# Kernel tuning notes

Hardware: AMD Instinct MI355X
Metric: run time of the kernel (lower is better)

Reference implementation:

```python
import jax, jax.numpy as jnp
import numpy as np

B = 65536
HID = 128
OUT = 10


def setup_inputs() -> dict:
    key = jax.random.key(0)
    ks = jax.random.split(key, 6)
    x = jax.random.normal(ks[0], (B, 784), dtype=jnp.float32)
    conv_w = jax.random.normal(ks[1], (3, 3), dtype=jnp.float32)
    # torch Linear(676,128): weight [128,676], bias [128]
    w1 = jax.random.normal(ks[2], (HID, 26 * 26), dtype=jnp.float32) * (1.0 / np.sqrt(26 * 26))
    b1 = jax.random.normal(ks[3], (HID,), dtype=jnp.float32) * 0.01
    w2 = jax.random.normal(ks[4], (OUT, HID), dtype=jnp.float32) * (1.0 / np.sqrt(HID))
    b2 = jax.random.normal(ks[5], (OUT,), dtype=jnp.float32) * 0.01
    return {"x": x, "conv_w": conv_w, "w1": w1, "b1": b1, "w2": w2, "b2": b2}


def reference(x, conv_w, w1, b1, w2, b2):
    b = x.shape[0]
    img = x.reshape(b, 1, 28, 28)                      # NCHW, single channel
    kern = conv_w.reshape(1, 1, 3, 3)                  # OIHW
    # valid 3x3 cross-correlation (matches the elementwise-multiply-and-sum loop)
    conv = jax.lax.conv_general_dilated(
        img, kern, window_strides=(1, 1), padding="VALID",
        dimension_numbers=("NCHW", "OIHW", "NCHW"))   # [B,1,26,26]
    feat = conv.reshape(b, 26 * 26)
    h = jax.nn.relu(feat @ w1.T + b1)                  # [B,128]
    return h @ w2.T + b2                               # [B,10]
```

## Files before the change

### kernel.cpp

```cpp
#include <hip/hip_runtime.h>
#include <hip/hip_bf16.h>

#define BATCH  65536
#define KREAL  784
#define BK     64
#define NCHUNK 13
#define HID    128
#define NOUT   10
#define BM     64
#define NTHR   256

using f32x4  = __attribute__((ext_vector_type(4))) float;
using short8 = __attribute__((ext_vector_type(8))) short;
using short4v= __attribute__((ext_vector_type(4))) short;
using f4     = __attribute__((ext_vector_type(4))) float;

__device__ inline short f2b(float f) {
    union { __hip_bfloat16 h; short s; } u;
    u.h = __float2bfloat16(f);
    return u.s;
}

#define GLDS16(gp, lp) \
    __builtin_amdgcn_global_load_lds((const __attribute__((address_space(1))) void*)(gp), \
                                     (__attribute__((address_space(3))) void*)(lp), 16, 0, 0)

#define NWB (NCHUNK*HID*BK)
#define NW2 (4*4*16*8)

__global__ void prep_kernel(const float* __restrict__ conv_w,
                            const float* __restrict__ w1,
                            const float* __restrict__ w2,
                            unsigned short* __restrict__ weff_sw,
                            unsigned short* __restrict__ w2f)
{
    int idx = blockIdx.x * 256 + threadIdx.x;
    if (idx < NWB) {
        int ic  = idx >> 13;
        int rem = idx & 8191;
        int r   = rem >> 6;
        int cc  = rem & 63;
        int g   = (cc >> 3) ^ (r & 7);
        int k   = ic * BK + g * 8 + (cc & 7);
        float acc = 0.f;
        if (k < KREAL) {
            int rr = k / 28, c = k - rr * 28;
            #pragma unroll
            for (int di = 0; di < 3; ++di) {
                int i = rr - di;
                if (i >= 0 && i < 26) {
                    #pragma unroll
                    for (int dj = 0; dj < 3; ++dj) {
                        int j = c - dj;
                        if (j >= 0 && j < 26)
                            acc = fmaf(w1[r * 676 + i * 26 + j], conv_w[di * 3 + dj], acc);
                    }
                }
            }
        }
        weff_sw[idx] = (unsigned short)f2b(acc);
    } else {
        int k2 = idx - NWB;
        if (k2 < NW2) {
            int e  = k2 & 7;
            int lo = (k2 >> 3) & 15;
            int hi = (k2 >> 7) & 3;
            int kk = k2 >> 9;
            float v = (lo < NOUT) ? w2[lo * HID + kk * 32 + hi * 8 + e] : 0.f;
            w2f[k2] = (unsigned short)f2b(v);
        }
    }
}

__global__ __launch_bounds__(NTHR, 4)
void fused_mlp_kernel(const float* __restrict__ x,
                      const float* __restrict__ b1,
                      const float* __restrict__ b2,
                      const unsigned short* __restrict__ weff_sw,
                      const unsigned short* __restrict__ w2f,
                      float* __restrict__ out)
{
    __shared__ __align__(16) unsigned char smem[40960];
    unsigned short* ldsA  = (unsigned short*)smem;
    unsigned short* ldsB0 = (unsigned short*)(smem + 8192);
    unsigned short* ldsB1 = (unsigned short*)(smem + 24576);
    unsigned short* ldsH  = (unsigned short*)smem;
    float*          outS  = (float*)(smem + 16384);

    const int tid  = threadIdx.x;
    const int wv   = tid >> 6;
    const int lane = tid & 63;
    const int lo   = lane & 15;
    const int hi   = lane >> 4;
    const int row0 = blockIdx.x * BM;
    const int wr0  = wv * 16;
    const int c0   = blockIdx.x % NCHUNK;

    f32x4 acc[8];
    #pragma unroll
    for (int t = 0; t < 8; ++t) acc[t] = (f32x4){0.f, 0.f, 0.f, 0.f};

    const char* abase = (const char*)(x + (long)(row0 + wr0 + hi) * KREAL);
    f4 av[4];
    auto issueA = [&](int ic) {
        #pragma unroll
        for (int j = 0; j < 4; ++j) {
            int ce = ic * BK + lo * 4;
            int cb = (ce + 4 <= KREAL) ? ce : 0;
            av[j] = *(const f4*)(abase + (long)j * 4 * KREAL * 4 + (long)cb * 4);
        }
    };
    auto writeA = [&]() {
        #pragma unroll
        for (int j = 0; j < 4; ++j) {
            int r = wr0 + j * 4 + hi;
            short4v c;
            c[0] = f2b(av[j][0]); c[1] = f2b(av[j][1]);
            c[2] = f2b(av[j][2]); c[3] = f2b(av[j][3]);
            int byteoff = r * 128 + ((((lo >> 1) ^ (r & 7)) << 4)) + ((lo & 1) << 3);
            *(short4v*)((char*)ldsA + byteoff) = c;
        }
    };
    auto stageB = [&](int ic, unsigned short* dst) {
        const char* src = (const char*)(weff_sw + (long)ic * (HID * BK));
        #pragma unroll
        for (int j = 0; j < 4; ++j)
            GLDS16(src + wv * 4096 + j * 1024 + lane * 16,
                   (char*)dst + wv * 4096 + j * 1024);
    };

    issueA(c0);
    stageB(c0, ldsB0);
    writeA();
    asm volatile("s_waitcnt vmcnt(0)" ::: "memory");
    __builtin_amdgcn_sched_barrier(0);
    __builtin_amdgcn_s_barrier();
    __builtin_amdgcn_sched_barrier(0);

    #pragma unroll
    for (int s = 0; s < NCHUNK; ++s) {
        int ic  = c0 + s;     if (ic >= NCHUNK)  ic -= NCHUNK;
        int icn = ic + 1;     if (icn >= NCHUNK) icn -= NCHUNK;
        const unsigned short* Bc = (s & 1) ? ldsB1 : ldsB0;
        if (s + 1 < NCHUNK) {
            issueA(icn);
            stageB(icn, (s & 1) ? ldsB0 : ldsB1);
        }
        const int r = wr0 + lo;
        #pragma unroll
        for (int kk = 0; kk < 2; ++kk) {
            const int G = kk * 4 + hi;
            short8 af = *(const short8*)((const char*)ldsA + r * 128 + ((G ^ (r & 7)) << 4));
            #pragma unroll
            for (int t = 0; t < 8; ++t) {
                const int ob = t * 16 + lo;
                short8 bfrag = *(const short8*)&Bc[ob * BK + ((G ^ (ob & 7)) << 3)];
                acc[t] = __builtin_amdgcn_mfma_f32_16x16x32_bf16(af, bfrag, acc[t], 0, 0, 0);
            }
        }
        if (s + 1 < NCHUNK) {
            __builtin_amdgcn_sched_barrier(0);
            writeA();
            __builtin_amdgcn_sched_barrier(0);
            asm volatile("s_waitcnt vmcnt(0)" ::: "memory");
            __builtin_amdgcn_sched_barrier(0);
            __builtin_amdgcn_s_barrier();
            __builtin_amdgcn_sched_barrier(0);
        }
    }

    __builtin_amdgcn_sched_barrier(0);
    __builtin_amdgcn_s_barrier();
    __builtin_amdgcn_sched_barrier(0);

    #pragma unroll
    for (int t = 0; t < 8; ++t) {
        float bias = b1[t * 16 + lo];
        #pragma unroll
        for (int j = 0; j < 4; ++j) {
            float hv = acc[t][j] + bias;
            hv = hv > 0.f ? hv : 0.f;
            int rloc = wr0 + hi * 4 + j;
            int col  = t * 16 + lo;
            int g    = col >> 3, e = col & 7;
            ldsH[rloc * HID + ((g ^ (rloc & 7)) << 3) + e] = (unsigned short)f2b(hv);
        }
    }

    f32x4 acc2 = (f32x4){0.f, 0.f, 0.f, 0.f};
    #pragma unroll
    for (int kk = 0; kk < 4; ++kk) {
        int r = wr0 + lo;
        int g = kk * 4 + hi;
        short8 ha = *(const short8*)&ldsH[r * HID + ((g ^ (r & 7)) << 3)];
        short8 wb = *(const short8*)(w2f + (((kk * 4 + hi) * 16 + lo) << 3));
        acc2 = __builtin_amdgcn_mfma_f32_16x16x32_bf16(ha, wb, acc2, 0, 0, 0);
    }
    float* os = outS + wv * 160;
    if (lo < NOUT) {
        float bb = b2[lo];
        #pragma unroll
        for (int j = 0; j < 4; ++j)
            os[(hi * 4 + j) * NOUT + lo] = acc2[j] + bb;
    }
    if (lane < 40) {
        f4 v = *(const f4*)&os[lane * 4];
        *(f4*)(out + (long)(row0 + wr0) * NOUT + lane * 4) = v;
    }
}

extern "C" void kernel_launch(void* const* d_in, const int* in_sizes, int n_in,
                              void* d_out, int out_size, void* d_ws, size_t ws_size,
                              hipStream_t stream)
{
    const float* x      = (const float*)d_in[0];
    const float* conv_w = (const float*)d_in[1];
    const float* w1     = (const float*)d_in[2];
    const float* b1     = (const float*)d_in[3];
    const float* w2     = (const float*)d_in[4];
    const float* b2     = (const float*)d_in[5];
    float* out = (float*)d_out;

    unsigned short* weff_sw = (unsigned short*)d_ws;
    unsigned short* w2f     = weff_sw + NWB;

    const int prep_total = NWB + NW2;
    prep_kernel<<<(prep_total + 255) / 256, 256, 0, stream>>>(conv_w, w1, w2, weff_sw, w2f);
    fused_mlp_kernel<<<BATCH / BM, NTHR, 0, stream>>>(x, b1, b2, weff_sw, w2f, out);
}
```

Baseline: 43.29 us.

## Split K across wave pairs with 512 threads and reduce partials in LDS

Doubles the block to 512 threads so each 16-row group is handled by two waves, each covering half of every 64-wide K chunk. The loads per thread for A and B staging are halved. At the end, one wave writes its partial hidden accumulators to LDS as bf16 and the other adds them before the bias, ReLU and the second layer. The goal is more waves in flight to hide memory latency. The cost is an extra LDS reduction and barrier, and bf16 rounding of the partial sums, which adds numerical error.

```diff
diff --git a/kernel.cpp b/kernel.cpp
--- a/kernel.cpp
+++ b/kernel.cpp
@@ -8,7 +8,7 @@
 #define HID    128
 #define NOUT   10
 #define BM     64
-#define NTHR   256
+#define NTHR   512
 
 using f32x4  = __attribute__((ext_vector_type(4))) float;
 using short8 = __attribute__((ext_vector_type(8))) short;
@@ -19,6 +19,10 @@
     union { __hip_bfloat16 h; short s; } u;
     u.h = __float2bfloat16(f);
     return u.s;
+}
+__device__ inline float b2f(unsigned short s) {
+    union { unsigned int u; float f; } c; c.u = ((unsigned int)s) << 16;
+    return c.f;
 }
 
 #define GLDS16(gp, lp) \
@@ -72,7 +76,7 @@
     }
 }
 
-__global__ __launch_bounds__(NTHR, 4)
+__global__ __launch_bounds__(NTHR, 7)
 void fused_mlp_kernel(const float* __restrict__ x,
                       const float* __restrict__ b1,
                       const float* __restrict__ b2,
@@ -85,48 +89,52 @@
     unsigned short* ldsB0 = (unsigned short*)(smem + 8192);
     unsigned short* ldsB1 = (unsigned short*)(smem + 24576);
     unsigned short* ldsH  = (unsigned short*)smem;
-    float*          outS  = (float*)(smem + 16384);
+    unsigned short* scrP  = (unsigned short*)(smem + 16384);
+    float*          outS  = (float*)(smem + 32768);
 
     const int tid  = threadIdx.x;
     const int wv   = tid >> 6;
     const int lane = tid & 63;
     const int lo   = lane & 15;
     const int hi   = lane >> 4;
+    const int g    = wv >> 1;
+    const int kh   = wv & 1;
     const int row0 = blockIdx.x * BM;
-    const int wr0  = wv * 16;
+    const int wr0  = g * 16;
     const int c0   = blockIdx.x % NCHUNK;
 
     f32x4 acc[8];
     #pragma unroll
     for (int t = 0; t < 8; ++t) acc[t] = (f32x4){0.f, 0.f, 0.f, 0.f};
 
-    const char* abase = (const char*)(x + (long)(row0 + wr0 + hi) * KREAL);
-    f4 av[4];
+    const char* abase = (const char*)(x + (long)(row0 + wr0 + (lane >> 3)) * KREAL);
+    f4 av[2];
     auto issueA = [&](int ic) {
         #pragma unroll
-        for (int j = 0; j < 4; ++j) {
-            int ce = ic * BK + lo * 4;
+        for (int j = 0; j < 2; ++j) {
+            int ce = ic * BK + kh * 32 + (lane & 7) * 4;
             int cb = (ce + 4 <= KREAL) ? ce : 0;
-            av[j] = *(const f4*)(abase + (long)j * 4 * KREAL * 4 + (long)cb * 4);
+            av[j] = *(const f4*)(abase + (long)j * 8 * KREAL * 4 + (long)cb * 4);
         }
     };
     auto writeA = [&]() {
         #pragma unroll
-        for (int j = 0; j < 4; ++j) {
-            int r = wr0 + j * 4 + hi;
+        for (int j = 0; j < 2; ++j) {
+            int r  = wr0 + j * 8 + (lane >> 3);
+            int cg = kh * 4 + ((lane & 7) >> 1);
             short4v c;
             c[0] = f2b(av[j][0]); c[1] = f2b(av[j][1]);
             c[2] = f2b(av[j][2]); c[3] = f2b(av[j][3]);
-            int byteoff = r * 128 + ((((lo >> 1) ^ (r & 7)) << 4)) + ((lo & 1) << 3);
-            *(short4v*)((char*)ldsA + byteoff) = c;
+            int off = r * 128 + ((cg ^ (r & 7)) << 4) + ((lane & 1) << 3);
+            *(short4v*)((char*)ldsA + off) = c;
         }
     };
     auto stageB = [&](int ic, unsigned short* dst) {
         const char* src = (const char*)(weff_sw + (long)ic * (HID * BK));
         #pragma unroll
-        for (int j = 0; j < 4; ++j)
-            GLDS16(src + wv * 4096 + j * 1024 + lane * 16,
-                   (char*)dst + wv * 4096 + j * 1024);
+        for (int j = 0; j < 2; ++j)
+            GLDS16(src + wv * 2048 + j * 1024 + lane * 16,
+                   (char*)dst + wv * 2048 + j * 1024);
     };
 
     issueA(c0);
@@ -146,10 +154,9 @@
             issueA(icn);
             stageB(icn, (s & 1) ? ldsB0 : ldsB1);
         }
-        const int r = wr0 + lo;
-        #pragma unroll
-        for (int kk = 0; kk < 2; ++kk) {
-            const int G = kk * 4 + hi;
+        {
+            const int r = wr0 + lo;
+            const int G = kh * 4 + hi;
             short8 af = *(const short8*)((const char*)ldsA + r * 128 + ((G ^ (r & 7)) << 4));
             #pragma unroll
             for (int t = 0; t < 8; ++t) {
@@ -173,39 +180,51 @@
     __builtin_amdgcn_s_barrier();
     __builtin_amdgcn_sched_barrier(0);
 
-    #pragma unroll
-    for (int t = 0; t < 8; ++t) {
-        float bias = b1[t * 16 + lo];
-        #pragma unroll
-        for (int j = 0; j < 4; ++j) {
-            float hv = acc[t][j] + bias;
-            hv = hv > 0.f ? hv : 0.f;
-            int rloc = wr0 + hi * 4 + j;
-            int col  = t * 16 + lo;
-            int g    = col >> 3, e = col & 7;
-            ldsH[rloc * HID + ((g ^ (rloc & 7)) << 3) + e] = (unsigned short)f2b(hv);
-        }
-    }
-
-    f32x4 acc2 = (f32x4){0.f, 0.f, 0.f, 0.f};
-    #pragma unroll
-    for (int kk = 0; kk < 4; ++kk) {
-        int r = wr0 + lo;
-        int g = kk * 4 + hi;
-        short8 ha = *(const short8*)&ldsH[r * HID + ((g ^ (r & 7)) << 3)];
-        short8 wb = *(const short8*)(w2f + (((kk * 4 + hi) * 16 + lo) << 3));
-        acc2 = __builtin_amdgcn_mfma_f32_16x16x32_bf16(ha, wb, acc2, 0, 0, 0);
-    }
-    float* os = outS + wv * 160;
-    if (lo < NOUT) {
-        float bb = b2[lo];
-        #pragma unroll
-        for (int j = 0; j < 4; ++j)
-            os[(hi * 4 + j) * NOUT + lo] = acc2[j] + bb;
-    }
-    if (lane < 40) {
-        f4 v = *(const f4*)&os[lane * 4];
-        *(f4*)(out + (long)(row0 + wr0) * NOUT + lane * 4) = v;
+    unsigned short* scr = scrP + g * 2048;
+    if (kh == 1) {
+        #pragma unroll
+        for (int t = 0; t < 8; ++t)
+            #pragma unroll
+            for (int j = 0; j < 4; ++j)
+                scr[(hi * 4 + j) * 128 + t * 16 + lo] = (unsigned short)f2b(acc[t][j]);
+    }
+    __syncthreads();
+
+    if (kh == 0) {
+        #pragma unroll
+        for (int t = 0; t < 8; ++t) {
+            float bias = b1[t * 16 + lo];
+            #pragma unroll
+            for (int j = 0; j < 4; ++j) {
+                float hv = acc[t][j] + b2f(scr[(hi * 4 + j) * 128 + t * 16 + lo]) + bias;
+                hv = hv > 0.f ? hv : 0.f;
+                int rloc = wr0 + hi * 4 + j;
+                int col  = t * 16 + lo;
+                int gg   = col >> 3, e = col & 7;
+                ldsH[rloc * HID + ((gg ^ (rloc & 7)) << 3) + e] = (unsigned short)f2b(hv);
+            }
+        }
+
+        f32x4 acc2 = (f32x4){0.f, 0.f, 0.f, 0.f};
+        #pragma unroll
+        for (int kk = 0; kk < 4; ++kk) {
+            int r  = wr0 + lo;
+            int gg = kk * 4 + hi;
+            short8 ha = *(const short8*)&ldsH[r * HID + ((gg ^ (r & 7)) << 3)];
+            short8 wb = *(const short8*)(w2f + (((kk * 4 + hi) * 16 + lo) << 3));
+            acc2 = __builtin_amdgcn_mfma_f32_16x16x32_bf16(ha, wb, acc2, 0, 0, 0);
+        }
+        float* os = outS + g * 160;
+        if (lo < NOUT) {
+            float bb = b2[lo];
+            #pragma unroll
+            for (int j = 0; j < 4; ++j)
+                os[(hi * 4 + j) * NOUT + lo] = acc2[j] + bb;
+        }
+        if (lane < 40) {
+            f4 v = *(const f4*)&os[lane * 4];
+            *(f4*)(out + (long)(row0 + wr0) * NOUT + lane * 4) = v;
+        }
     }
 }
 
```

Measured after the change: 48.45 us. +11.9%, slower.

## Prefetch A two chunks ahead in registers and single-buffer B in LDS

Applied to the files above, without the earlier changes.

Restructures the K-loop pipeline. A tiles are now loaded into registers two chunks ahead and double-buffered in LDS, while the weight tile B goes into a single LDS buffer that is staged each iteration just before use. The goal is to hide global latency of x loads better and cut LDS use from 40KB to 32KB, which may allow more resident blocks. In exchange, B loads are no longer overlapped with the previous chunk's MFMAs, so each iteration waits on the B fetch before computing.

```diff
diff --git a/kernel.cpp b/kernel.cpp
--- a/kernel.cpp
+++ b/kernel.cpp
@@ -80,10 +80,10 @@
                       const unsigned short* __restrict__ w2f,
                       float* __restrict__ out)
 {
-    __shared__ __align__(16) unsigned char smem[40960];
-    unsigned short* ldsA  = (unsigned short*)smem;
-    unsigned short* ldsB0 = (unsigned short*)(smem + 8192);
-    unsigned short* ldsB1 = (unsigned short*)(smem + 24576);
+    __shared__ __align__(16) unsigned char smem[32768];
+    unsigned short* ldsA0 = (unsigned short*)smem;
+    unsigned short* ldsA1 = (unsigned short*)(smem + 8192);
+    unsigned short* ldsB  = (unsigned short*)(smem + 16384);
     unsigned short* ldsH  = (unsigned short*)smem;
     float*          outS  = (float*)(smem + 16384);
 
@@ -101,68 +101,78 @@
     for (int t = 0; t < 8; ++t) acc[t] = (f32x4){0.f, 0.f, 0.f, 0.f};
 
     const char* abase = (const char*)(x + (long)(row0 + wr0 + hi) * KREAL);
-    f4 av[4];
-    auto issueA = [&](int ic) {
+    f4 av0[4], av1[4];
+    auto issueA = [&](int ic, f4 (&v)[4]) {
         #pragma unroll
         for (int j = 0; j < 4; ++j) {
             int ce = ic * BK + lo * 4;
             int cb = (ce + 4 <= KREAL) ? ce : 0;
-            av[j] = *(const f4*)(abase + (long)j * 4 * KREAL * 4 + (long)cb * 4);
+            v[j] = *(const f4*)(abase + (long)j * 4 * KREAL * 4 + (long)cb * 4);
         }
     };
-    auto writeA = [&]() {
+    auto writeA = [&](f4 (&v)[4], unsigned short* dstA) {
         #pragma unroll
         for (int j = 0; j < 4; ++j) {
             int r = wr0 + j * 4 + hi;
             short4v c;
-            c[0] = f2b(av[j][0]); c[1] = f2b(av[j][1]);
-            c[2] = f2b(av[j][2]); c[3] = f2b(av[j][3]);
+            c[0] = f2b(v[j][0]); c[1] = f2b(v[j][1]);
+            c[2] = f2b(v[j][2]); c[3] = f2b(v[j][3]);
             int byteoff = r * 128 + ((((lo >> 1) ^ (r & 7)) << 4)) + ((lo & 1) << 3);
-            *(short4v*)((char*)ldsA + byteoff) = c;
+            *(short4v*)((char*)dstA + byteoff) = c;
         }
     };
-    auto stageB = [&](int ic, unsigned short* dst) {
+    auto stageB = [&](int ic) {
         const char* src = (const char*)(weff_sw + (long)ic * (HID * BK));
         #pragma unroll
         for (int j = 0; j < 4; ++j)
             GLDS16(src + wv * 4096 + j * 1024 + lane * 16,
-                   (char*)dst + wv * 4096 + j * 1024);
+                   (char*)ldsB + wv * 4096 + j * 1024);
     };
 
-    issueA(c0);
-    stageB(c0, ldsB0);
-    writeA();
-    asm volatile("s_waitcnt vmcnt(0)" ::: "memory");
-    __builtin_amdgcn_sched_barrier(0);
-    __builtin_amdgcn_s_barrier();
-    __builtin_amdgcn_sched_barrier(0);
+    {
+        int c1 = (c0 + 1 < NCHUNK) ? c0 + 1 : c0 + 1 - NCHUNK;
+        issueA(c0, av0);
+        issueA(c1, av1);
+        asm volatile("s_waitcnt vmcnt(4)" ::: "memory");
+        __builtin_amdgcn_sched_barrier(0);
+        writeA(av0, ldsA0);
+        __builtin_amdgcn_sched_barrier(0);
+    }
 
     #pragma unroll
     for (int s = 0; s < NCHUNK; ++s) {
-        int ic  = c0 + s;     if (ic >= NCHUNK)  ic -= NCHUNK;
-        int icn = ic + 1;     if (icn >= NCHUNK) icn -= NCHUNK;
-        const unsigned short* Bc = (s & 1) ? ldsB1 : ldsB0;
-        if (s + 1 < NCHUNK) {
-            issueA(icn);
-            stageB(icn, (s & 1) ? ldsB0 : ldsB1);
-        }
+        int ic  = c0 + s;      if (ic  >= NCHUNK) ic  -= NCHUNK;
+        int ic2 = ic + 2;      if (ic2 >= NCHUNK) ic2 -= NCHUNK;
+        const unsigned short* Acur = (s & 1) ? ldsA1 : ldsA0;
+        unsigned short*       Anxt = (s & 1) ? ldsA0 : ldsA1;
+
+        stageB(ic);
+        if (s + 2 < NCHUNK) {
+            if (s & 1) issueA(ic2, av1); else issueA(ic2, av0);
+            asm volatile("s_waitcnt vmcnt(4)" ::: "memory");
+        } else {
+            asm volatile("s_waitcnt vmcnt(0)" ::: "memory");
+        }
+        __builtin_amdgcn_sched_barrier(0);
+        __builtin_amdgcn_s_barrier();
+        __builtin_amdgcn_sched_barrier(0);
+
         const int r = wr0 + lo;
         #pragma unroll
         for (int kk = 0; kk < 2; ++kk) {
             const int G = kk * 4 + hi;
-            short8 af = *(const short8*)((const char*)ldsA + r * 128 + ((G ^ (r & 7)) << 4));
+            short8 af = *(const short8*)((const char*)Acur + r * 128 + ((G ^ (r & 7)) << 4));
             #pragma unroll
             for (int t = 0; t < 8; ++t) {
                 const int ob = t * 16 + lo;
-                short8 bfrag = *(const short8*)&Bc[ob * BK + ((G ^ (ob & 7)) << 3)];
+                short8 bfrag = *(const short8*)&ldsB[ob * BK + ((G ^ (ob & 7)) << 3)];
                 acc[t] = __builtin_amdgcn_mfma_f32_16x16x32_bf16(af, bfrag, acc[t], 0, 0, 0);
             }
         }
+
         if (s + 1 < NCHUNK) {
             __builtin_amdgcn_sched_barrier(0);
-            writeA();
-            __builtin_amdgcn_sched_barrier(0);
-            asm volatile("s_waitcnt vmcnt(0)" ::: "memory");
+            if (s & 1) writeA(av0, Anxt); else writeA(av1, Anxt);
             __builtin_amdgcn_sched_barrier(0);
             __builtin_amdgcn_s_barrier();
             __builtin_amdgcn_sched_barrier(0);
```

Result: no change. 43.94 us (+1.5%).
